# Kernel optimization log

Hardware: AMD Instinct MI355X
Metric: run time of the kernel (lower is better)

## Reference

```python
import jax, jax.numpy as jnp
import numpy as np

NUM_HEADS = 8
GROUPS = 32
EPS = 1e-5


def group_norm(x, gamma, beta):
    # x: (b, c, L)
    b, c, L = x.shape
    xg = x.reshape(b, GROUPS, c // GROUPS, L)
    mean = xg.mean(axis=(2, 3), keepdims=True)
    var = xg.var(axis=(2, 3), keepdims=True)
    xn = ((xg - mean) / jnp.sqrt(var + EPS)).reshape(b, c, L)
    return xn * gamma[None, :, None] + beta[None, :, None]


def setup_inputs() -> dict:
    key = jax.random.key(0)
    ks = jax.random.split(key, 8)
    b, c, h, w = 8, 512, 32, 32
    inner = c  # inner_channels == -1 -> channels
    x = jax.random.normal(ks[0], (b, c, h, w), dtype=jnp.float32)
    gamma = jnp.ones((c,), dtype=jnp.float32)
    beta = jnp.zeros((c,), dtype=jnp.float32)
    Wq = jax.random.normal(ks[1], (inner, c), dtype=jnp.float32) * 0.02
    bq = jnp.zeros((inner,), dtype=jnp.float32)
    Wkv = jax.random.normal(ks[2], (2 * inner, c), dtype=jnp.float32) * 0.02
    bkv = jnp.zeros((2 * inner,), dtype=jnp.float32)
    Wo = jax.random.normal(ks[3], (c, inner), dtype=jnp.float32) * 0.02
    bo = jnp.zeros((c,), dtype=jnp.float32)
    return {"x": x, "gamma": gamma, "beta": beta, "Wq": Wq, "bq": bq,
            "Wkv": Wkv, "bkv": bkv, "Wo": Wo, "bo": bo}


def reference(x, gamma, beta, Wq, bq, Wkv, bkv, Wo, bo):
    b, c = x.shape[:2]
    spatial = x.shape[2:]
    L = int(np.prod(spatial))
    inner = Wq.shape[0]
    dh = inner // NUM_HEADS
    scale = dh ** -0.5  # NOTE: applied to BOTH q and k, as in the source

    xr = x.reshape(b, c, L)
    hn = group_norm(xr, gamma, beta)          # norm(x); also serves as context

    # 1x1 Conv1d == channel matmul
    q = jnp.einsum('oc,bcl->bol', Wq, hn) + bq[None, :, None]
    kv = jnp.einsum('oc,bcl->bol', Wkv, hn) + bkv[None, :, None]
    k, v = jnp.split(kv, 2, axis=1)

    # (b, heads, dh, L)
    qh = (q * scale).reshape(b, NUM_HEADS, dh, L)
    kh = (k * scale).reshape(b, NUM_HEADS, dh, L)
    vh = v.reshape(b, NUM_HEADS, dh, L)

    dots = jnp.einsum('bhdt,bhds->bhts', qh, kh)
    attn = jax.nn.softmax(dots.astype(jnp.float32), axis=-1).astype(dots.dtype)
    out = jnp.einsum('bhts,bhds->bhdt', attn, vh)  # (b, heads, dh, L)

    out = out.reshape(b, inner, L)
    # output Linear over the channel dim
    out = jnp.einsum('oc,bcl->bol', Wo, out) + bo[None, :, None]
    return (xr + out).reshape(b, c, *spatial)
```

## Files before the change

kernel.cpp:

```cpp
#include <hip/hip_runtime.h>
#include <math.h>

#define B_ 8
#define C_ 512
#define L_ 1024
#define NH_ 8
#define DH_ 64
#define EPS 1e-5f
#define SCALE 0.125f
#define QSCALE (0.125f * 1.44269504088896f)

typedef __bf16 bf16x8 __attribute__((ext_vector_type(8)));
typedef __bf16 bf16x4 __attribute__((ext_vector_type(4)));
typedef float  f32x4  __attribute__((ext_vector_type(4)));

#define MFMA16(a, b, c) __builtin_amdgcn_mfma_f32_16x16x32_bf16((a), (b), (c), 0, 0, 0)

__device__ __forceinline__ void glds16(const __bf16* g, __bf16* l) {
    __builtin_amdgcn_global_load_lds((const __attribute__((address_space(1))) void*)(g),
                                     (__attribute__((address_space(3))) void*)(l),
                                     16, 0, 0);
}

__global__ __launch_bounds__(256)
void wconvert_kernel(const float* __restrict__ Wq, const float* __restrict__ Wkv,
                     const float* __restrict__ Wo, __bf16* __restrict__ dst) {
    int idx = blockIdx.x * 256 + threadIdx.x;
    float4 v;
    if (idx < 65536)        v = ((const float4*)Wq)[idx];
    else if (idx < 196608)  v = ((const float4*)Wkv)[idx - 65536];
    else                    v = ((const float4*)Wo)[idx - 196608];
    bf16x4 o;
    o[0] = (__bf16)v.x; o[1] = (__bf16)v.y; o[2] = (__bf16)v.z; o[3] = (__bf16)v.w;
    ((bf16x4*)dst)[idx] = o;
}

__global__ __launch_bounds__(256)
void gn_kernel(const float* __restrict__ x, const float* __restrict__ gamma,
               const float* __restrict__ beta, __bf16* __restrict__ hnT) {
    int bg = blockIdx.x;
    int b = bg >> 5, g = bg & 31;
    size_t goff = ((size_t)b * C_ + (size_t)g * 16) * L_;
    const float4* x4 = (const float4*)(x + goff);
    int tid = threadIdx.x;

    float s = 0.f, ss = 0.f;
    for (int i = tid; i < 4096; i += 256) {
        float4 v = x4[i];
        s  += v.x + v.y + v.z + v.w;
        ss += v.x * v.x + v.y * v.y + v.z * v.z + v.w * v.w;
    }
    __shared__ float rs[256], rss[256];
    rs[tid] = s; rss[tid] = ss;
    __syncthreads();
    for (int off = 128; off > 0; off >>= 1) {
        if (tid < off) { rs[tid] += rs[tid + off]; rss[tid] += rss[tid + off]; }
        __syncthreads();
    }
    const float inv_n = 1.f / 16384.f;
    float mean = rs[0] * inv_n;
    float var  = rss[0] * inv_n - mean * mean;
    float rstd = rsqrtf(var + EPS);

    for (int it = 0; it < 4; ++it) {
        int l = tid + it * 256;
        bf16x8 p0, p1;
#pragma unroll
        for (int j = 0; j < 16; ++j) {
            float v = x[goff + (size_t)j * L_ + l];
            float y = (v - mean) * (gamma[g * 16 + j] * rstd) + beta[g * 16 + j];
            if (j < 8) p0[j] = (__bf16)y; else p1[j - 8] = (__bf16)y;
        }
        size_t o = ((size_t)b * L_ + l) * C_ + g * 16;
        *(bf16x8*)&hnT[o]     = p0;
        *(bf16x8*)&hnT[o + 8] = p1;
    }
}

__device__ __forceinline__
void gemm_mainloop(const __bf16* __restrict__ A, const __bf16* __restrict__ Bp,
                   __bf16* As, __bf16* Bs, f32x4 acc[4][4]) {
    const int tid = threadIdx.x;
    const int lane = tid & 63, w = tid >> 6;
    const int c = lane & 15, q = lane >> 4;
    const int wm = (w >> 1) * 64, wn = (w & 1) * 64;
    const int l8 = lane >> 3, kgsw = (lane & 7) ^ l8;

    for (int k0 = 0; k0 < 512; k0 += 64) {
#pragma unroll
        for (int i = 0; i < 4; ++i) {
            int chunk = w * 4 + i;
            int row = chunk * 8 + l8;
            glds16(A  + (size_t)row * 512 + k0 + kgsw * 8, &As[chunk * 512]);
            glds16(Bp + (size_t)row * 512 + k0 + kgsw * 8, &Bs[chunk * 512]);
        }
        __syncthreads();
#pragma unroll
        for (int ks = 0; ks < 2; ++ks) {
            const int koff = ((ks * 4 + q) ^ (c & 7)) * 8;
            bf16x8 af[4], bfr[4];
#pragma unroll
            for (int m = 0; m < 4; ++m)
                af[m] = *(const bf16x8*)&As[(wm + m * 16 + c) * 64 + koff];
#pragma unroll
            for (int n = 0; n < 4; ++n)
                bfr[n] = *(const bf16x8*)&Bs[(wn + n * 16 + c) * 64 + koff];
#pragma unroll
            for (int m = 0; m < 4; ++m)
#pragma unroll
                for (int n = 0; n < 4; ++n)
                    acc[m][n] = MFMA16(af[m], bfr[n], acc[m][n]);
        }
        __syncthreads();
    }
}

__global__ __launch_bounds__(256)
void qkv_kernel(const __bf16* __restrict__ Wq_bf, const __bf16* __restrict__ Wkv_bf,
                const __bf16* __restrict__ hnT,
                const float* __restrict__ bq, const float* __restrict__ bkv,
                __bf16* __restrict__ qT, __bf16* __restrict__ kT,
                __bf16* __restrict__ vv) {
    __shared__ __bf16 As[128 * 64], Bs[128 * 64];
    const int b = blockIdx.y;
    const int xx = blockIdx.x;
    const int sec = xx >> 5, t = xx & 31;
    const __bf16* hb = hnT + (size_t)b * L_ * C_;

    const __bf16 *A, *Bp;
    int m0, n0;
    if (sec < 2) {
        m0 = (t & 3) * 128; n0 = (t >> 2) * 128;
        A  = (sec == 0 ? Wq_bf : Wkv_bf) + (size_t)m0 * 512;
        Bp = hb + (size_t)n0 * 512;
    } else {
        m0 = (t >> 2) * 128; n0 = (t & 3) * 128;
        A  = hb + (size_t)m0 * 512;
        Bp = Wkv_bf + (size_t)(512 + n0) * 512;
    }

    f32x4 acc[4][4];
#pragma unroll
    for (int m = 0; m < 4; ++m)
#pragma unroll
        for (int n = 0; n < 4; ++n)
#pragma unroll
            for (int r = 0; r < 4; ++r) acc[m][n][r] = 0.f;

    gemm_mainloop(A, Bp, As, Bs, acc);

    const int tid = threadIdx.x, lane = tid & 63, w = tid >> 6;
    const int c = lane & 15, q = lane >> 4;
    const int wm = (w >> 1) * 64, wn = (w & 1) * 64;

    if (sec < 2) {
        const float* bias = (sec == 0) ? bq : bkv;
        const float scl = (sec == 0) ? QSCALE : SCALE;
        __bf16* dst = (sec == 0) ? qT : kT;
#pragma unroll
        for (int mt = 0; mt < 4; ++mt)
#pragma unroll
            for (int nt = 0; nt < 4; ++nt) {
                int ob = m0 + wm + mt * 16 + q * 4;
                int l  = n0 + wn + nt * 16 + c;
                int h = ob >> 6, d0 = ob & 63;
                bf16x4 ov;
#pragma unroll
                for (int r = 0; r < 4; ++r)
                    ov[r] = (__bf16)((acc[mt][nt][r] + bias[ob + r]) * scl);
                *(bf16x4*)&dst[((size_t)(b * NH_ + h) * L_ + l) * DH_ + d0] = ov;
            }
    } else {
#pragma unroll
        for (int mt = 0; mt < 4; ++mt)
#pragma unroll
            for (int nt = 0; nt < 4; ++nt) {
                int lb = m0 + wm + mt * 16 + q * 4;
                int o  = n0 + wn + nt * 16 + c;
                float bi = bkv[512 + o];
                bf16x4 ov;
#pragma unroll
                for (int r = 0; r < 4; ++r)
                    ov[r] = (__bf16)(acc[mt][nt][r] + bi);
                *(bf16x4*)&vv[((size_t)b * C_ + o) * L_ + lb] = ov;
            }
    }
}

__global__ __launch_bounds__(256)
void attn_kernel(const __bf16* __restrict__ qT, const __bf16* __restrict__ kT,
                 const __bf16* __restrict__ vv, __bf16* __restrict__ aoT) {
    const int tt = blockIdx.x, h = blockIdx.y, b = blockIdx.z;
    const int t0 = tt * 64;
    __shared__ __bf16 Qs[64 * 64], Ks[64 * 64], Vs[64 * 64], Ps[64 * 64];

    const int tid = threadIdx.x, lane = tid & 63, w = tid >> 6;
    const int c = lane & 15, q = lane >> 4;
    const int l8 = lane >> 3, kgsw = (lane & 7) ^ l8;

    const __bf16* qbase = qT + ((size_t)(b * NH_ + h) * L_ + t0) * DH_;
    const __bf16* kbase = kT + (size_t)(b * NH_ + h) * L_ * DH_;
    const __bf16* vbase = vv + (size_t)(b * C_ + h * DH_) * L_;

#pragma unroll
    for (int i = 0; i < 2; ++i) {
        int chunk = w * 2 + i;
        int row = chunk * 8 + l8;
        glds16(qbase + (size_t)row * DH_ + kgsw * 8, &Qs[chunk * 512]);
    }

    float l_run = 0.f;
    f32x4 o_acc[4];
#pragma unroll
    for (int dt = 0; dt < 4; ++dt)
#pragma unroll
        for (int r = 0; r < 4; ++r) o_acc[dt][r] = 0.f;

    for (int s0 = 0; s0 < L_; s0 += 64) {
#pragma unroll
        for (int i = 0; i < 2; ++i) {
            int chunk = w * 2 + i;
            int row = chunk * 8 + l8;
            glds16(kbase + (size_t)(s0 + row) * DH_ + kgsw * 8, &Ks[chunk * 512]);
            glds16(vbase + (size_t)row * L_ + s0 + kgsw * 8, &Vs[chunk * 512]);
        }
        __syncthreads();

        f32x4 sres[4];
#pragma unroll
        for (int mt = 0; mt < 4; ++mt)
#pragma unroll
            for (int r = 0; r < 4; ++r) sres[mt][r] = 0.f;
#pragma unroll
        for (int ks = 0; ks < 2; ++ks) {
            const int koff = ((ks * 4 + q) ^ (c & 7)) * 8;
            bf16x8 bq_ = *(const bf16x8*)&Qs[(w * 16 + c) * 64 + koff];
#pragma unroll
            for (int mt = 0; mt < 4; ++mt) {
                bf16x8 ak = *(const bf16x8*)&Ks[(mt * 16 + c) * 64 + koff];
                sres[mt] = MFMA16(ak, bq_, sres[mt]);
            }
        }

        float ps = 0.f;
#pragma unroll
        for (int mt = 0; mt < 4; ++mt) {
            bf16x4 pv;
#pragma unroll
            for (int r = 0; r < 4; ++r) {
                float p = exp2f(sres[mt][r]);
                ps += p;
                pv[r] = (__bf16)p;
            }
            int u = (mt * 4 + q) ^ ((c & 7) << 1);
            *(bf16x4*)&Ps[(w * 16 + c) * 64 + u * 4] = pv;
        }
        ps += __shfl_xor(ps, 16);
        ps += __shfl_xor(ps, 32);
        l_run += ps;

#pragma unroll
        for (int ks = 0; ks < 2; ++ks) {
            const int up = ((ks * 8 + q * 2) ^ ((c & 7) << 1)) * 4;
            bf16x8 bp = *(const bf16x8*)&Ps[(w * 16 + c) * 64 + up];
            const int koff = ((ks * 4 + q) ^ (c & 7)) * 8;
#pragma unroll
            for (int dt = 0; dt < 4; ++dt) {
                bf16x8 av = *(const bf16x8*)&Vs[(dt * 16 + c) * 64 + koff];
                o_acc[dt] = MFMA16(av, bp, o_acc[dt]);
            }
        }
        __syncthreads();
    }

    float linv = 1.f / l_run;
    __bf16* aobase = aoT + ((size_t)b * L_ + t0 + w * 16 + c) * C_ + h * DH_;
#pragma unroll
    for (int dt = 0; dt < 4; ++dt) {
        bf16x4 ov;
#pragma unroll
        for (int r = 0; r < 4; ++r) ov[r] = (__bf16)(o_acc[dt][r] * linv);
        *(bf16x4*)&aobase[dt * 16 + q * 4] = ov;
    }
}

__global__ __launch_bounds__(256)
void proj_kernel(const __bf16* __restrict__ aoT, const __bf16* __restrict__ Wo_bf,
                 const float* __restrict__ bo, const float* __restrict__ x,
                 float* __restrict__ out) {
    __shared__ __bf16 As[128 * 64], Bs[128 * 64];
    const int b = blockIdx.y, t = blockIdx.x;
    const int m0 = (t >> 2) * 128;
    const int n0 = (t & 3) * 128;
    const __bf16* A  = aoT + (size_t)b * L_ * C_ + (size_t)m0 * 512;
    const __bf16* Bp = Wo_bf + (size_t)n0 * 512;

    f32x4 acc[4][4];
#pragma unroll
    for (int m = 0; m < 4; ++m)
#pragma unroll
        for (int n = 0; n < 4; ++n)
#pragma unroll
            for (int r = 0; r < 4; ++r) acc[m][n][r] = 0.f;

    gemm_mainloop(A, Bp, As, Bs, acc);

    const int tid = threadIdx.x, lane = tid & 63, w = tid >> 6;
    const int c = lane & 15, q = lane >> 4;
    const int wm = (w >> 1) * 64, wn = (w & 1) * 64;

#pragma unroll
    for (int mt = 0; mt < 4; ++mt)
#pragma unroll
        for (int nt = 0; nt < 4; ++nt) {
            int lb = m0 + wm + mt * 16 + q * 4;
            int o  = n0 + wn + nt * 16 + c;
            float bi = bo[o];
            size_t off = ((size_t)b * C_ + o) * L_ + lb;
            float4 xv = *(const float4*)&x[off];
            float4 rv;
            rv.x = acc[mt][nt][0] + bi + xv.x;
            rv.y = acc[mt][nt][1] + bi + xv.y;
            rv.z = acc[mt][nt][2] + bi + xv.z;
            rv.w = acc[mt][nt][3] + bi + xv.w;
            *(float4*)&out[off] = rv;
        }
}

extern "C" void kernel_launch(void* const* d_in, const int* in_sizes, int n_in,
                              void* d_out, int out_size, void* d_ws, size_t ws_size,
                              hipStream_t stream) {
    const float* x     = (const float*)d_in[0];
    const float* gamma = (const float*)d_in[1];
    const float* beta  = (const float*)d_in[2];
    const float* Wq    = (const float*)d_in[3];
    const float* bq    = (const float*)d_in[4];
    const float* Wkv   = (const float*)d_in[5];
    const float* bkv   = (const float*)d_in[6];
    const float* Wo    = (const float*)d_in[7];
    const float* bo    = (const float*)d_in[8];
    float* out = (float*)d_out;

    __bf16* wsb = (__bf16*)d_ws;
    __bf16* Wq_bf  = wsb;
    __bf16* Wkv_bf = wsb + 262144;
    __bf16* Wo_bf  = wsb + 786432;
    __bf16* hnT    = wsb + 1048576;
    __bf16* qT     = wsb + 5242880;
    __bf16* kT     = wsb + 9437184;
    __bf16* vv     = wsb + 13631488;
    __bf16* aoT    = wsb + 17825792;

    wconvert_kernel<<<dim3(1024), 256, 0, stream>>>(Wq, Wkv, Wo, wsb);
    gn_kernel<<<dim3(B_ * 32), 256, 0, stream>>>(x, gamma, beta, hnT);
    qkv_kernel<<<dim3(96, B_), 256, 0, stream>>>(Wq_bf, Wkv_bf, hnT, bq, bkv, qT, kT, vv);
    attn_kernel<<<dim3(16, NH_, B_), 256, 0, stream>>>(qT, kT, vv, aoT);
    proj_kernel<<<dim3(32, B_), 256, 0, stream>>>(aoT, Wo_bf, bo, x, out);
}
```

Baseline: 175.7 us.

## Split GroupNorm, stage QKV epilogue via LDS, widen attention query tile

Several changes at once. The weight conversion and the GroupNorm statistics now run in one prep kernel. A separate GroupNorm apply kernel transposes through LDS so its global reads and writes are coalesced. The QKV epilogue stages its output tile through shared memory so each thread stores 16-byte vectors. The attention kernel now handles 128 queries per block so each K/V tile is reused twice as often, and it computes the softmax row sums with an MFMA against a ones matrix instead of shuffles. The cost is more LDS and registers per block in attention, and half as many attention blocks.

```diff
diff --git a/kernel.cpp b/kernel.cpp
--- a/kernel.cpp
+++ b/kernel.cpp
@@ -23,57 +23,74 @@
 }
 
 __global__ __launch_bounds__(256)
-void wconvert_kernel(const float* __restrict__ Wq, const float* __restrict__ Wkv,
-                     const float* __restrict__ Wo, __bf16* __restrict__ dst) {
-    int idx = blockIdx.x * 256 + threadIdx.x;
-    float4 v;
-    if (idx < 65536)        v = ((const float4*)Wq)[idx];
-    else if (idx < 196608)  v = ((const float4*)Wkv)[idx - 65536];
-    else                    v = ((const float4*)Wo)[idx - 196608];
-    bf16x4 o;
-    o[0] = (__bf16)v.x; o[1] = (__bf16)v.y; o[2] = (__bf16)v.z; o[3] = (__bf16)v.w;
-    ((bf16x4*)dst)[idx] = o;
-}
-
-__global__ __launch_bounds__(256)
-void gn_kernel(const float* __restrict__ x, const float* __restrict__ gamma,
-               const float* __restrict__ beta, __bf16* __restrict__ hnT) {
-    int bg = blockIdx.x;
-    int b = bg >> 5, g = bg & 31;
-    size_t goff = ((size_t)b * C_ + (size_t)g * 16) * L_;
+void prep_kernel(const float* __restrict__ Wq, const float* __restrict__ Wkv,
+                 const float* __restrict__ Wo, __bf16* __restrict__ dst,
+                 const float* __restrict__ x, float* __restrict__ stats) {
+    __shared__ float rs[256], rss[256];
+    int bid = blockIdx.x, tid = threadIdx.x;
+    if (bid < 1024) {
+        int idx = bid * 256 + tid;
+        float4 v;
+        if (idx < 65536)        v = ((const float4*)Wq)[idx];
+        else if (idx < 196608)  v = ((const float4*)Wkv)[idx - 65536];
+        else                    v = ((const float4*)Wo)[idx - 196608];
+        bf16x4 o;
+        o[0] = (__bf16)v.x; o[1] = (__bf16)v.y; o[2] = (__bf16)v.z; o[3] = (__bf16)v.w;
+        ((bf16x4*)dst)[idx] = o;
+        return;
+    }
+    int bg = bid - 1024;
+    size_t goff = (size_t)bg * 16 * L_;
     const float4* x4 = (const float4*)(x + goff);
-    int tid = threadIdx.x;
-
     float s = 0.f, ss = 0.f;
     for (int i = tid; i < 4096; i += 256) {
         float4 v = x4[i];
         s  += v.x + v.y + v.z + v.w;
         ss += v.x * v.x + v.y * v.y + v.z * v.z + v.w * v.w;
     }
-    __shared__ float rs[256], rss[256];
     rs[tid] = s; rss[tid] = ss;
     __syncthreads();
     for (int off = 128; off > 0; off >>= 1) {
         if (tid < off) { rs[tid] += rs[tid + off]; rss[tid] += rss[tid + off]; }
         __syncthreads();
     }
-    const float inv_n = 1.f / 16384.f;
-    float mean = rs[0] * inv_n;
-    float var  = rss[0] * inv_n - mean * mean;
-    float rstd = rsqrtf(var + EPS);
-
-    for (int it = 0; it < 4; ++it) {
-        int l = tid + it * 256;
-        bf16x8 p0, p1;
-#pragma unroll
-        for (int j = 0; j < 16; ++j) {
-            float v = x[goff + (size_t)j * L_ + l];
-            float y = (v - mean) * (gamma[g * 16 + j] * rstd) + beta[g * 16 + j];
-            if (j < 8) p0[j] = (__bf16)y; else p1[j - 8] = (__bf16)y;
-        }
-        size_t o = ((size_t)b * L_ + l) * C_ + g * 16;
-        *(bf16x8*)&hnT[o]     = p0;
-        *(bf16x8*)&hnT[o + 8] = p1;
+    if (tid == 0) {
+        const float inv_n = 1.f / 16384.f;
+        float mean = rs[0] * inv_n;
+        float var  = rss[0] * inv_n - mean * mean;
+        stats[bg * 2]     = mean;
+        stats[bg * 2 + 1] = rsqrtf(var + EPS);
+    }
+}
+
+__global__ __launch_bounds__(256)
+void gn_apply_kernel(const float* __restrict__ x, const float* __restrict__ gamma,
+                     const float* __restrict__ beta, const float* __restrict__ stats,
+                     __bf16* __restrict__ hnT) {
+    __shared__ __bf16 T[32 * 520];
+    const int lt = blockIdx.x, b = blockIdx.y;
+    const int tid = threadIdx.x;
+    const int l0 = lt * 32;
+    const int cbase = tid >> 3, fl = tid & 7;
+#pragma unroll
+    for (int p = 0; p < 16; ++p) {
+        int cc = cbase + p * 32;
+        float4 v = *(const float4*)&x[((size_t)b * C_ + cc) * L_ + l0 + fl * 4];
+        int bg = b * 32 + (cc >> 4);
+        float m = stats[bg * 2], rstd = stats[bg * 2 + 1];
+        float ga = gamma[cc] * rstd, be = beta[cc];
+        T[(fl * 4 + 0) * 520 + cc] = (__bf16)((v.x - m) * ga + be);
+        T[(fl * 4 + 1) * 520 + cc] = (__bf16)((v.y - m) * ga + be);
+        T[(fl * 4 + 2) * 520 + cc] = (__bf16)((v.z - m) * ga + be);
+        T[(fl * 4 + 3) * 520 + cc] = (__bf16)((v.w - m) * ga + be);
+    }
+    __syncthreads();
+    const int lrow = tid >> 6, cu = tid & 63;
+#pragma unroll
+    for (int pp = 0; pp < 8; ++pp) {
+        int l = pp * 4 + lrow;
+        bf16x8 r = *(const bf16x8*)&T[l * 520 + cu * 8];
+        *(bf16x8*)&hnT[((size_t)b * L_ + l0 + l) * C_ + cu * 8] = r;
     }
 }
 
@@ -121,7 +138,9 @@
                 const float* __restrict__ bq, const float* __restrict__ bkv,
                 __bf16* __restrict__ qT, __bf16* __restrict__ kT,
                 __bf16* __restrict__ vv) {
-    __shared__ __bf16 As[128 * 64], Bs[128 * 64];
+    __shared__ __bf16 SMEM[128 * 64 * 2];
+    __bf16* As = SMEM;
+    __bf16* Bs = SMEM + 128 * 64;
     const int b = blockIdx.y;
     const int xx = blockIdx.x;
     const int sec = xx >> 5, t = xx & 31;
@@ -153,37 +172,48 @@
     const int c = lane & 15, q = lane >> 4;
     const int wm = (w >> 1) * 64, wn = (w & 1) * 64;
 
-    if (sec < 2) {
-        const float* bias = (sec == 0) ? bq : bkv;
-        const float scl = (sec == 0) ? QSCALE : SCALE;
-        __bf16* dst = (sec == 0) ? qT : kT;
-#pragma unroll
-        for (int mt = 0; mt < 4; ++mt)
-#pragma unroll
-            for (int nt = 0; nt < 4; ++nt) {
+    __bf16* T2 = SMEM;
+    const float* bias = (sec == 0) ? bq : bkv;
+    const float scl = (sec == 0) ? QSCALE : SCALE;
+#pragma unroll
+    for (int mt = 0; mt < 4; ++mt)
+#pragma unroll
+        for (int nt = 0; nt < 4; ++nt) {
+            int n_loc = wn + nt * 16 + c;
+            int u4 = (wm >> 2) + mt * 4 + q;
+            int u4sw = u4 ^ ((n_loc & 7) << 1);
+            bf16x4 ov;
+            if (sec < 2) {
                 int ob = m0 + wm + mt * 16 + q * 4;
-                int l  = n0 + wn + nt * 16 + c;
-                int h = ob >> 6, d0 = ob & 63;
-                bf16x4 ov;
 #pragma unroll
                 for (int r = 0; r < 4; ++r)
                     ov[r] = (__bf16)((acc[mt][nt][r] + bias[ob + r]) * scl);
-                *(bf16x4*)&dst[((size_t)(b * NH_ + h) * L_ + l) * DH_ + d0] = ov;
-            }
-    } else {
-#pragma unroll
-        for (int mt = 0; mt < 4; ++mt)
-#pragma unroll
-            for (int nt = 0; nt < 4; ++nt) {
-                int lb = m0 + wm + mt * 16 + q * 4;
-                int o  = n0 + wn + nt * 16 + c;
-                float bi = bkv[512 + o];
-                bf16x4 ov;
+            } else {
+                float bi = bkv[512 + n0 + n_loc];
 #pragma unroll
                 for (int r = 0; r < 4; ++r)
                     ov[r] = (__bf16)(acc[mt][nt][r] + bi);
-                *(bf16x4*)&vv[((size_t)b * C_ + o) * L_ + lb] = ov;
             }
+            *(bf16x4*)&T2[n_loc * 128 + u4sw * 4] = ov;
+        }
+    __syncthreads();
+#pragma unroll
+    for (int p = 0; p < 8; ++p) {
+        int rrow = p * 16 + (tid >> 4);
+        int u16 = tid & 15;
+        int u4p = (u16 * 2) ^ ((rrow & 7) << 1);
+        bf16x8 val = *(const bf16x8*)&T2[rrow * 128 + u4p * 4];
+        if (sec < 2) {
+            int l = n0 + rrow;
+            int og = m0 + u16 * 8;
+            int hh = og >> 6, d0 = og & 63;
+            __bf16* dstp = (sec == 0) ? qT : kT;
+            *(bf16x8*)&dstp[((size_t)(b * NH_ + hh) * L_ + l) * DH_ + d0] = val;
+        } else {
+            int o = n0 + rrow;
+            int lg = m0 + u16 * 8;
+            *(bf16x8*)&vv[((size_t)b * C_ + o) * L_ + lg] = val;
+        }
     }
 }
 
@@ -191,96 +221,120 @@
 void attn_kernel(const __bf16* __restrict__ qT, const __bf16* __restrict__ kT,
                  const __bf16* __restrict__ vv, __bf16* __restrict__ aoT) {
     const int tt = blockIdx.x, h = blockIdx.y, b = blockIdx.z;
-    const int t0 = tt * 64;
-    __shared__ __bf16 Qs[64 * 64], Ks[64 * 64], Vs[64 * 64], Ps[64 * 64];
+    const int t0 = tt * 128;
+    __shared__ __bf16 Qs[128 * 64];
+    __shared__ __bf16 Ks[64 * 64];
+    __shared__ __bf16 Vs[64 * 64];
+    __shared__ __bf16 Ones[16 * 64];
+    __shared__ __bf16 Ps[128 * 72];
 
     const int tid = threadIdx.x, lane = tid & 63, w = tid >> 6;
     const int c = lane & 15, q = lane >> 4;
-    const int l8 = lane >> 3, kgsw = (lane & 7) ^ l8;
+    const int l8 = lane >> 3, kg = (lane & 7) ^ l8;
 
     const __bf16* qbase = qT + ((size_t)(b * NH_ + h) * L_ + t0) * DH_;
     const __bf16* kbase = kT + (size_t)(b * NH_ + h) * L_ * DH_;
     const __bf16* vbase = vv + (size_t)(b * C_ + h * DH_) * L_;
 
-#pragma unroll
-    for (int i = 0; i < 2; ++i) {
-        int chunk = w * 2 + i;
+    {
+        int row = tid >> 4, u8 = tid & 15;
+        int u8sw = (((u8 >> 1) ^ (row & 7)) << 1) | (u8 & 1);
+        float fv = (row == 0) ? 1.f : 0.f;
+        bf16x4 val;
+        val[0] = (__bf16)fv; val[1] = (__bf16)fv; val[2] = (__bf16)fv; val[3] = (__bf16)fv;
+        *(bf16x4*)&Ones[row * 64 + u8sw * 4] = val;
+    }
+#pragma unroll
+    for (int i = 0; i < 4; ++i) {
+        int chunk = w * 4 + i;
         int row = chunk * 8 + l8;
-        glds16(qbase + (size_t)row * DH_ + kgsw * 8, &Qs[chunk * 512]);
-    }
-
-    float l_run = 0.f;
-    f32x4 o_acc[4];
-#pragma unroll
-    for (int dt = 0; dt < 4; ++dt)
-#pragma unroll
-        for (int r = 0; r < 4; ++r) o_acc[dt][r] = 0.f;
+        glds16(qbase + (size_t)row * DH_ + kg * 8, &Qs[chunk * 512]);
+    }
+
+    f32x4 o_acc[2][4], o_l[2];
+#pragma unroll
+    for (int n2 = 0; n2 < 2; ++n2) {
+#pragma unroll
+        for (int dt = 0; dt < 4; ++dt)
+#pragma unroll
+            for (int r = 0; r < 4; ++r) o_acc[n2][dt][r] = 0.f;
+#pragma unroll
+        for (int r = 0; r < 4; ++r) o_l[n2][r] = 0.f;
+    }
 
     for (int s0 = 0; s0 < L_; s0 += 64) {
 #pragma unroll
         for (int i = 0; i < 2; ++i) {
             int chunk = w * 2 + i;
             int row = chunk * 8 + l8;
-            glds16(kbase + (size_t)(s0 + row) * DH_ + kgsw * 8, &Ks[chunk * 512]);
-            glds16(vbase + (size_t)row * L_ + s0 + kgsw * 8, &Vs[chunk * 512]);
+            glds16(kbase + (size_t)(s0 + row) * DH_ + kg * 8, &Ks[chunk * 512]);
+            glds16(vbase + (size_t)row * L_ + s0 + kg * 8, &Vs[chunk * 512]);
         }
         __syncthreads();
 
-        f32x4 sres[4];
+        f32x4 sres[4][2];
 #pragma unroll
         for (int mt = 0; mt < 4; ++mt)
 #pragma unroll
-            for (int r = 0; r < 4; ++r) sres[mt][r] = 0.f;
+            for (int r = 0; r < 4; ++r) { sres[mt][0][r] = 0.f; sres[mt][1][r] = 0.f; }
 #pragma unroll
         for (int ks = 0; ks < 2; ++ks) {
             const int koff = ((ks * 4 + q) ^ (c & 7)) * 8;
-            bf16x8 bq_ = *(const bf16x8*)&Qs[(w * 16 + c) * 64 + koff];
+            bf16x8 bQ0 = *(const bf16x8*)&Qs[(w * 32 + c) * 64 + koff];
+            bf16x8 bQ1 = *(const bf16x8*)&Qs[(w * 32 + 16 + c) * 64 + koff];
 #pragma unroll
             for (int mt = 0; mt < 4; ++mt) {
-                bf16x8 ak = *(const bf16x8*)&Ks[(mt * 16 + c) * 64 + koff];
-                sres[mt] = MFMA16(ak, bq_, sres[mt]);
+                bf16x8 aK = *(const bf16x8*)&Ks[(mt * 16 + c) * 64 + koff];
+                sres[mt][0] = MFMA16(aK, bQ0, sres[mt][0]);
+                sres[mt][1] = MFMA16(aK, bQ1, sres[mt][1]);
             }
         }
 
-        float ps = 0.f;
-#pragma unroll
-        for (int mt = 0; mt < 4; ++mt) {
-            bf16x4 pv;
-#pragma unroll
-            for (int r = 0; r < 4; ++r) {
-                float p = exp2f(sres[mt][r]);
-                ps += p;
-                pv[r] = (__bf16)p;
+#pragma unroll
+        for (int n2 = 0; n2 < 2; ++n2) {
+            int trow = w * 32 + n2 * 16 + c;
+#pragma unroll
+            for (int mt = 0; mt < 4; ++mt) {
+                bf16x4 pv;
+#pragma unroll
+                for (int r = 0; r < 4; ++r) pv[r] = (__bf16)exp2f(sres[mt][n2][r]);
+                *(bf16x4*)&Ps[trow * 72 + (mt * 4 + q) * 4] = pv;
             }
-            int u = (mt * 4 + q) ^ ((c & 7) << 1);
-            *(bf16x4*)&Ps[(w * 16 + c) * 64 + u * 4] = pv;
-        }
-        ps += __shfl_xor(ps, 16);
-        ps += __shfl_xor(ps, 32);
-        l_run += ps;
+        }
 
 #pragma unroll
         for (int ks = 0; ks < 2; ++ks) {
-            const int up = ((ks * 8 + q * 2) ^ ((c & 7) << 1)) * 4;
-            bf16x8 bp = *(const bf16x8*)&Ps[(w * 16 + c) * 64 + up];
             const int koff = ((ks * 4 + q) ^ (c & 7)) * 8;
-#pragma unroll
-            for (int dt = 0; dt < 4; ++dt) {
-                bf16x8 av = *(const bf16x8*)&Vs[(dt * 16 + c) * 64 + koff];
-                o_acc[dt] = MFMA16(av, bp, o_acc[dt]);
+            bf16x8 aV[4];
+#pragma unroll
+            for (int dt = 0; dt < 4; ++dt)
+                aV[dt] = *(const bf16x8*)&Vs[(dt * 16 + c) * 64 + koff];
+            bf16x8 aO = *(const bf16x8*)&Ones[c * 64 + koff];
+#pragma unroll
+            for (int n2 = 0; n2 < 2; ++n2) {
+                bf16x8 bp = *(const bf16x8*)&Ps[(w * 32 + n2 * 16 + c) * 72 + ks * 32 + q * 8];
+#pragma unroll
+                for (int dt = 0; dt < 4; ++dt)
+                    o_acc[n2][dt] = MFMA16(aV[dt], bp, o_acc[n2][dt]);
+                o_l[n2] = MFMA16(aO, bp, o_l[n2]);
             }
         }
         __syncthreads();
     }
 
-    float linv = 1.f / l_run;
-    __bf16* aobase = aoT + ((size_t)b * L_ + t0 + w * 16 + c) * C_ + h * DH_;
-#pragma unroll
-    for (int dt = 0; dt < 4; ++dt) {
-        bf16x4 ov;
-#pragma unroll
-        for (int r = 0; r < 4; ++r) ov[r] = (__bf16)(o_acc[dt][r] * linv);
-        *(bf16x4*)&aobase[dt * 16 + q * 4] = ov;
+#pragma unroll
+    for (int n2 = 0; n2 < 2; ++n2) {
+        float lsum = __shfl(o_l[n2][0], c);
+        float linv = 1.f / lsum;
+        int tg = t0 + w * 32 + n2 * 16 + c;
+        __bf16* aobase = aoT + ((size_t)b * L_ + tg) * C_ + h * DH_;
+#pragma unroll
+        for (int dt = 0; dt < 4; ++dt) {
+            bf16x4 ov;
+#pragma unroll
+            for (int r = 0; r < 4; ++r) ov[r] = (__bf16)(o_acc[n2][dt][r] * linv);
+            *(bf16x4*)&aobase[dt * 16 + q * 4] = ov;
+        }
     }
 }
 
@@ -350,10 +404,11 @@
     __bf16* kT     = wsb + 9437184;
     __bf16* vv     = wsb + 13631488;
     __bf16* aoT    = wsb + 17825792;
-
-    wconvert_kernel<<<dim3(1024), 256, 0, stream>>>(Wq, Wkv, Wo, wsb);
-    gn_kernel<<<dim3(B_ * 32), 256, 0, stream>>>(x, gamma, beta, hnT);
+    float*  stats  = (float*)(wsb + 22020096);
+
+    prep_kernel<<<dim3(1280), 256, 0, stream>>>(Wq, Wkv, Wo, wsb, x, stats);
+    gn_apply_kernel<<<dim3(32, B_), 256, 0, stream>>>(x, gamma, beta, stats, hnT);
     qkv_kernel<<<dim3(96, B_), 256, 0, stream>>>(Wq_bf, Wkv_bf, hnT, bq, bkv, qT, kT, vv);
-    attn_kernel<<<dim3(16, NH_, B_), 256, 0, stream>>>(qT, kT, vv, aoT);
+    attn_kernel<<<dim3(8, NH_, B_), 256, 0, stream>>>(qT, kT, vv, aoT);
     proj_kernel<<<dim3(32, B_), 256, 0, stream>>>(aoT, Wo_bf, bo, x, out);
 }
```

New measurement: 172.4 us. About the same (-1.9%).
